# Kernel optimization log

Hardware: AMD Instinct MI355X
Metric: run time of the kernel (lower is better)

## Reference

```python
import jax, jax.numpy as jnp
import numpy as np

LN_EPS = 1e-5


def setup_inputs() -> dict:
    key = jax.random.key(0)
    ks = jax.random.split(key, 6)
    B, I, H = 16384, 512, 512
    x = jax.random.normal(ks[0], (B, I), dtype=jnp.float32)
    h_prev = jax.random.normal(ks[1], (B, H), dtype=jnp.float32)
    c_prev = jax.random.normal(ks[2], (B, H), dtype=jnp.float32)
    # packed gate weights in i|f|g|o order (equivalent to 8 separate matmuls)
    W_i = jax.random.normal(ks[3], (I, 4 * H), dtype=jnp.float32) * (1.0 / np.sqrt(I))
    W_h = jax.random.normal(ks[4], (H, 4 * H), dtype=jnp.float32) * (1.0 / np.sqrt(H))
    # biases: b_i=0, b_f=1, b_g=0, b_o=0 as in the torch module
    b = jnp.concatenate([jnp.zeros(H), jnp.ones(H), jnp.zeros(H), jnp.zeros(H)]).astype(jnp.float32)
    ln_weight = jnp.ones((H,), dtype=jnp.float32)
    ln_bias = jnp.zeros((H,), dtype=jnp.float32)
    return {"x": x, "h_prev": h_prev, "c_prev": c_prev, "W_i": W_i, "W_h": W_h,
            "b": b, "ln_weight": ln_weight, "ln_bias": ln_bias}


def layer_norm(h, w, bias):
    mu = jnp.mean(h, axis=-1, keepdims=True)
    var = jnp.var(h, axis=-1, keepdims=True)
    return (h - mu) * jax.lax.rsqrt(var + LN_EPS) * w + bias


def reference(x, h_prev, c_prev, W_i, W_h, b, ln_weight, ln_bias):
    H = h_prev.shape[-1]
    # two fused GEMMs covering all 4 gates: [B, 4H]
    gates = x @ W_i + h_prev @ W_h + b
    i, f, g, o = jnp.split(gates, 4, axis=-1)
    i = jax.nn.sigmoid(i)
    f = jax.nn.sigmoid(f)
    g = jnp.tanh(g)
    o = jax.nn.sigmoid(o)
    c = f * c_prev + i * g
    h = o * jnp.tanh(c)
    h = layer_norm(h, ln_weight, ln_bias)
    return (h, c)
```

## Files before the change

### kernel.cpp

```cpp
#include <hip/hip_runtime.h>
#include <cstdint>
#include <cstddef>

typedef unsigned short ushort_t;
typedef __attribute__((ext_vector_type(8))) short bf16x8;
typedef __attribute__((ext_vector_type(4))) float f32x4;

#define MROWS 16384
#define KDIM  1024
#define NDIM  2048
#define HDIM  512
#define NTILE 16

static __device__ __forceinline__ unsigned short f2bf(float f) {
    unsigned int u = __float_as_uint(f);
    u += 0x7fffu + ((u >> 16) & 1u);
    return (unsigned short)(u >> 16);
}

static __device__ __forceinline__ float sigmoid_f(float x) {
    return 1.0f / (1.0f + __expf(-x));
}
static __device__ __forceinline__ float tanh_f(float x) {
    float t = __expf(2.0f * x);
    return 1.0f - 2.0f / (t + 1.0f);
}

__global__ __launch_bounds__(256) void pack_ab(const float* __restrict__ x,
                                               const float* __restrict__ hp,
                                               const float* __restrict__ Wi,
                                               const float* __restrict__ Wh,
                                               ushort_t* __restrict__ A,
                                               ushort_t* __restrict__ Bt) {
    __shared__ ushort_t sm[64][72];
    const int tid = threadIdx.x;
    if (blockIdx.x < 8192) {
        int t = blockIdx.x * 256 + tid;
        int row = t >> 7;
        int kc = (t & 127) << 3;
        const float* src = (kc < 512) ? (x + (size_t)row * 512 + kc)
                                      : (hp + (size_t)row * 512 + (kc - 512));
        float4 v0 = ((const float4*)src)[0];
        float4 v1 = ((const float4*)src)[1];
        ushort_t o[8] __attribute__((aligned(16)));
        o[0] = f2bf(v0.x); o[1] = f2bf(v0.y); o[2] = f2bf(v0.z); o[3] = f2bf(v0.w);
        o[4] = f2bf(v1.x); o[5] = f2bf(v1.y); o[6] = f2bf(v1.z); o[7] = f2bf(v1.w);
        *((uint4*)(A + (size_t)row * KDIM + kc)) = *((const uint4*)o);
    } else {
        int b2 = blockIdx.x - 8192;
        int kt = b2 >> 5;
        int ct = b2 & 31;
        const float* W = (kt < 8) ? (Wi + (size_t)(kt * 64) * NDIM)
                                  : (Wh + (size_t)((kt - 8) * 64) * NDIM);
        int c0 = (tid & 15) * 4;
        int r0 = tid >> 4;
#pragma unroll
        for (int r = 0; r < 4; ++r) {
            int krow = r * 16 + r0;
            float4 v = *((const float4*)(W + (size_t)krow * NDIM + ct * 64 + c0));
            sm[krow][c0 + 0] = f2bf(v.x);
            sm[krow][c0 + 1] = f2bf(v.y);
            sm[krow][c0 + 2] = f2bf(v.z);
            sm[krow][c0 + 3] = f2bf(v.w);
        }
        __syncthreads();
        int g = (ct * 64) >> 9;
        int h0 = ct * 64 - g * 512;
#pragma unroll
        for (int q = tid; q < 512; q += 256) {
            int cc = q >> 3;
            int kc = (q & 7) * 8;
            ushort_t o[8] __attribute__((aligned(16)));
#pragma unroll
            for (int j = 0; j < 8; ++j) o[j] = sm[kc + j][cc];
            int np = 4 * (h0 + cc) + g;
            *((uint4*)(Bt + (size_t)np * KDIM + kt * 64 + kc)) = *((const uint4*)o);
        }
    }
}

__global__ __launch_bounds__(512, 2) void gemm_cell(const ushort_t* __restrict__ A,
                                                    const ushort_t* __restrict__ Bt,
                                                    const float* __restrict__ b,
                                                    const float* __restrict__ c_prev,
                                                    float* __restrict__ h_out,
                                                    float* __restrict__ c_out) {
    __shared__ ushort_t lds[2][32768];

    const int tid  = threadIdx.x;
    const int w    = tid >> 6;
    const int lane = tid & 63;
    const int mi   = w >> 2;
    const int nj   = w & 3;
    int bid = blockIdx.x;
    int lid = (bid & 7) * 64 + (bid >> 3);
    const int m0 = (lid >> 3) * 256;
    const int n0 = (lid & 7) * 256;
    const int lr   = lane & 15;
    const int quad = lane >> 4;
    const int sw   = lr & 7;

    const int trow0 = tid >> 3;
    const int chg   = (tid & 7) ^ (trow0 & 7);
    const size_t a_base = (size_t)(m0 + trow0) * KDIM + chg * 8;
    const size_t b_base = (size_t)(n0 + trow0) * KDIM + chg * 8;
    const int    l_base = tid * 16;

#define STAGE_A(kt, bufi) do {                                                      \
    const ushort_t* ap_ = A + a_base + (size_t)(kt) * 64;                           \
    char* al_ = (char*)&lds[bufi][0];                                               \
    _Pragma("unroll")                                                               \
    for (int r_ = 0; r_ < 4; ++r_)                                                  \
        __builtin_amdgcn_global_load_lds(                                           \
            (const __attribute__((address_space(1))) void*)(ap_ + (size_t)r_ * 64 * KDIM), \
            (__attribute__((address_space(3))) void*)(al_ + l_base + r_ * 8192),    \
            16, 0, 0);                                                              \
} while (0)
#define STAGE_B(kt, bufi) do {                                                      \
    const ushort_t* bp_ = Bt + b_base + (size_t)(kt) * 64;                          \
    char* bl_ = (char*)&lds[bufi][16384];                                           \
    _Pragma("unroll")                                                               \
    for (int r_ = 0; r_ < 4; ++r_)                                                  \
        __builtin_amdgcn_global_load_lds(                                           \
            (const __attribute__((address_space(1))) void*)(bp_ + (size_t)r_ * 64 * KDIM), \
            (__attribute__((address_space(3))) void*)(bl_ + l_base + r_ * 8192),    \
            16, 0, 0);                                                              \
} while (0)

    f32x4 acc[8][4];
#pragma unroll
    for (int i = 0; i < 8; ++i)
#pragma unroll
        for (int j = 0; j < 4; ++j) acc[i][j] = (f32x4){0.f, 0.f, 0.f, 0.f};

    STAGE_A(0, 0); STAGE_B(0, 0);
    STAGE_A(1, 1); STAGE_B(1, 1);
    asm volatile("s_waitcnt vmcnt(8)\n\ts_barrier" ::: "memory");

#define TILE(t_, BUF_) do {                                                         \
    const ushort_t* Ab_ = &lds[BUF_][0];                                            \
    const ushort_t* Bb_ = &lds[BUF_][16384];                                        \
    bf16x8 af[4][2], b0v[2][2], b1v[2][2];                                          \
                                 \
    _Pragma("unroll")                                                               \
    for (int t2 = 0; t2 < 4; ++t2) {                                                \
        int ra = mi * 128 + t2 * 16 + lr;                                           \
        af[t2][0] = *((const bf16x8*)(Ab_ + (ra * 8 + (quad ^ sw)) * 8));           \
        af[t2][1] = *((const bf16x8*)(Ab_ + (ra * 8 + ((4 + quad) ^ sw)) * 8));     \
    }                                                                               \
    _Pragma("unroll")                                                               \
    for (int j = 0; j < 2; ++j) {                                                   \
        int rb = nj * 64 + j * 16 + lr;                                             \
        b0v[j][0] = *((const bf16x8*)(Bb_ + (rb * 8 + (quad ^ sw)) * 8));           \
        b0v[j][1] = *((const bf16x8*)(Bb_ + (rb * 8 + ((4 + quad) ^ sw)) * 8));     \
    }                                                                               \
    __builtin_amdgcn_s_barrier();                                                   \
    __builtin_amdgcn_s_setprio(1);                                                  \
    _Pragma("unroll")                                                               \
    for (int t2 = 0; t2 < 4; ++t2)                                                  \
        _Pragma("unroll")                                                           \
        for (int j = 0; j < 2; ++j) {                                               \
            acc[t2][j] = __builtin_amdgcn_mfma_f32_16x16x32_bf16(                   \
                af[t2][0], b0v[j][0], acc[t2][j], 0, 0, 0);                         \
            acc[t2][j] = __builtin_amdgcn_mfma_f32_16x16x32_bf16(                   \
                af[t2][1], b0v[j][1], acc[t2][j], 0, 0, 0);                         \
        }                                                                           \
    __builtin_amdgcn_s_setprio(0);                                                  \
    asm volatile("s_barrier" ::: "memory");                                         \
                                        \
    _Pragma("unroll")                                                               \
    for (int j = 0; j < 2; ++j) {                                                   \
        int rb = nj * 64 + (j + 2) * 16 + lr;                                       \
        b1v[j][0] = *((const bf16x8*)(Bb_ + (rb * 8 + (quad ^ sw)) * 8));           \
        b1v[j][1] = *((const bf16x8*)(Bb_ + (rb * 8 + ((4 + quad) ^ sw)) * 8));     \
    }                                                                               \
    __builtin_amdgcn_s_barrier();                                                   \
    __builtin_amdgcn_s_setprio(1);                                                  \
    _Pragma("unroll")                                                               \
    for (int t2 = 0; t2 < 4; ++t2)                                                  \
        _Pragma("unroll")                                                           \
        for (int j = 0; j < 2; ++j) {                                               \
            acc[t2][j + 2] = __builtin_amdgcn_mfma_f32_16x16x32_bf16(               \
                af[t2][0], b1v[j][0], acc[t2][j + 2], 0, 0, 0);                     \
            acc[t2][j + 2] = __builtin_amdgcn_mfma_f32_16x16x32_bf16(               \
                af[t2][1], b1v[j][1], acc[t2][j + 2], 0, 0, 0);                     \
        }                                                                           \
    __builtin_amdgcn_s_setprio(0);                                                  \
    asm volatile("s_barrier" ::: "memory");          \
                         \
    _Pragma("unroll")                                                               \
    for (int t2 = 0; t2 < 4; ++t2) {                                                \
        int ra = mi * 128 + (t2 + 4) * 16 + lr;                                     \
        af[t2][0] = *((const bf16x8*)(Ab_ + (ra * 8 + (quad ^ sw)) * 8));           \
        af[t2][1] = *((const bf16x8*)(Ab_ + (ra * 8 + ((4 + quad) ^ sw)) * 8));     \
    }                                                                               \
    if ((t_) < NTILE - 2) STAGE_B((t_) + 2, BUF_);                                  \
    __builtin_amdgcn_s_barrier();                                                   \
    __builtin_amdgcn_s_setprio(1);                                                  \
    _Pragma("unroll")                                                               \
    for (int t2 = 0; t2 < 4; ++t2)                                                  \
        _Pragma("unroll")                                                           \
        for (int j = 0; j < 2; ++j) {                                               \
            acc[t2 + 4][j + 2] = __builtin_amdgcn_mfma_f32_16x16x32_bf16(           \
                af[t2][0], b1v[j][0], acc[t2 + 4][j + 2], 0, 0, 0);                 \
            acc[t2 + 4][j + 2] = __builtin_amdgcn_mfma_f32_16x16x32_bf16(           \
                af[t2][1], b1v[j][1], acc[t2 + 4][j + 2], 0, 0, 0);                 \
        }                                                                           \
    __builtin_amdgcn_s_setprio(0);                                                  \
    asm volatile("s_barrier" ::: "memory");          \
                            \
    if ((t_) < NTILE - 2) STAGE_A((t_) + 2, BUF_);                                  \
    __builtin_amdgcn_s_barrier();                                                   \
    __builtin_amdgcn_s_setprio(1);                                                  \
    _Pragma("unroll")                                                               \
    for (int t2 = 0; t2 < 4; ++t2)                                                  \
        _Pragma("unroll")                                                           \
        for (int j = 0; j < 2; ++j) {                                               \
            acc[t2 + 4][j] = __builtin_amdgcn_mfma_f32_16x16x32_bf16(               \
                af[t2][0], b0v[j][0], acc[t2 + 4][j], 0, 0, 0);                     \
            acc[t2 + 4][j] = __builtin_amdgcn_mfma_f32_16x16x32_bf16(               \
                af[t2][1], b0v[j][1], acc[t2 + 4][j], 0, 0, 0);                     \
        }                                                                           \
    __builtin_amdgcn_s_setprio(0);                                                  \
    if ((t_) < NTILE - 2) {                                                         \
                 \
        asm volatile("s_waitcnt vmcnt(8)\n\ts_barrier" ::: "memory");               \
    } else if ((t_) == NTILE - 2) {                                                 \
        asm volatile("s_waitcnt vmcnt(0)\n\ts_barrier" ::: "memory");               \
    } else {                                                                        \
        asm volatile("s_waitcnt lgkmcnt(0)\n\ts_barrier" ::: "memory");             \
    }                                                                               \
} while (0)

    for (int tp = 0; tp < NTILE / 2; ++tp) {
        TILE(2 * tp, 0);
        TILE(2 * tp + 1, 1);
    }
#undef TILE
#undef STAGE_A
#undef STAGE_B

    float* scr = (float*)&lds[0][0] + w * 1024;
    const int rr = lane >> 2;
    const int hg0 = ((n0 + nj * 64) >> 2) + (lane & 3) * 4;
    const float4 bi4 = *((const float4*)(b + hg0));
    const float4 bff = *((const float4*)(b + 512 + hg0));
    const float4 bgg = *((const float4*)(b + 1024 + hg0));
    const float4 boo = *((const float4*)(b + 1536 + hg0));
    const float bi[4] = {bi4.x, bi4.y, bi4.z, bi4.w};
    const float bfv[4] = {bff.x, bff.y, bff.z, bff.w};
    const float bg[4] = {bgg.x, bgg.y, bgg.z, bgg.w};
    const float bo[4] = {boo.x, boo.y, boo.z, boo.w};

#pragma unroll
    for (int tm = 0; tm < 8; ++tm) {
#pragma unroll
        for (int tn = 0; tn < 4; ++tn) {
            int c = tn * 16 + lr;
#pragma unroll
            for (int rg = 0; rg < 4; ++rg) {
                int r = quad * 4 + rg;
                int blk = (c >> 2) ^ r;
                scr[r * 64 + blk * 4 + (c & 3)] = acc[tm][tn][rg];
            }
        }
        float4 gv[4];
#pragma unroll
        for (int j = 0; j < 4; ++j) {
            int cb = (lane & 3) * 4 + j;
            gv[j] = *((const float4*)(scr + rr * 64 + (cb ^ rr) * 4));
        }
        int grow = m0 + mi * 128 + tm * 16 + rr;
        float4 cp4 = *((const float4*)(c_prev + (size_t)grow * HDIM + hg0));
        const float cpv[4] = {cp4.x, cp4.y, cp4.z, cp4.w};
        float cn[4], hv[4];
#pragma unroll
        for (int j = 0; j < 4; ++j) {
            float iv = sigmoid_f(gv[j].x + bi[j]);
            float fv = sigmoid_f(gv[j].y + bfv[j]);
            float g2 = tanh_f(gv[j].z + bg[j]);
            float ov = sigmoid_f(gv[j].w + bo[j]);
            cn[j] = fv * cpv[j] + iv * g2;
            hv[j] = ov * tanh_f(cn[j]);
        }
        float4 cno = {cn[0], cn[1], cn[2], cn[3]};
        float4 hvo = {hv[0], hv[1], hv[2], hv[3]};
        *((float4*)(c_out + (size_t)grow * HDIM + hg0)) = cno;
        *((float4*)(h_out + (size_t)grow * HDIM + hg0)) = hvo;
    }
}

__global__ __launch_bounds__(256) void ln_kernel(float* __restrict__ h,
                                                 const float* __restrict__ lw,
                                                 const float* __restrict__ lb) {
    int w = threadIdx.x >> 6;
    int lane = threadIdx.x & 63;
    int row = blockIdx.x * 4 + w;
    float* p = h + (size_t)row * HDIM + lane * 8;
    float4 a = ((const float4*)p)[0];
    float4 c = ((const float4*)p)[1];
    float s  = a.x + a.y + a.z + a.w + c.x + c.y + c.z + c.w;
    float ss = a.x * a.x + a.y * a.y + a.z * a.z + a.w * a.w +
               c.x * c.x + c.y * c.y + c.z * c.z + c.w * c.w;
#pragma unroll
    for (int off = 32; off > 0; off >>= 1) {
        s  += __shfl_xor(s, off);
        ss += __shfl_xor(ss, off);
    }
    float mu = s * (1.0f / 512.0f);
    float var = ss * (1.0f / 512.0f) - mu * mu;
    float rstd = rsqrtf(var + 1e-5f);
    const float* wp = lw + lane * 8;
    const float* bp = lb + lane * 8;
    float4 w0 = ((const float4*)wp)[0];
    float4 w1 = ((const float4*)wp)[1];
    float4 b0 = ((const float4*)bp)[0];
    float4 b1 = ((const float4*)bp)[1];
    a.x = (a.x - mu) * rstd * w0.x + b0.x;
    a.y = (a.y - mu) * rstd * w0.y + b0.y;
    a.z = (a.z - mu) * rstd * w0.z + b0.z;
    a.w = (a.w - mu) * rstd * w0.w + b0.w;
    c.x = (c.x - mu) * rstd * w1.x + b1.x;
    c.y = (c.y - mu) * rstd * w1.y + b1.y;
    c.z = (c.z - mu) * rstd * w1.z + b1.z;
    c.w = (c.w - mu) * rstd * w1.w + b1.w;
    ((float4*)p)[0] = a;
    ((float4*)p)[1] = c;
}

extern "C" void kernel_launch(void* const* d_in, const int* in_sizes, int n_in,
                              void* d_out, int out_size, void* d_ws, size_t ws_size,
                              hipStream_t stream) {
    const float* x      = (const float*)d_in[0];
    const float* h_prev = (const float*)d_in[1];
    const float* c_prev = (const float*)d_in[2];
    const float* W_i    = (const float*)d_in[3];
    const float* W_h    = (const float*)d_in[4];
    const float* b      = (const float*)d_in[5];
    const float* ln_w   = (const float*)d_in[6];
    const float* ln_b   = (const float*)d_in[7];

    float* h_out = (float*)d_out;
    float* c_out = h_out + (size_t)MROWS * HDIM;

    ushort_t* A  = (ushort_t*)d_ws;
    ushort_t* Bt = A + (size_t)MROWS * KDIM;

    pack_ab<<<8192 + 512, 256, 0, stream>>>(x, h_prev, W_i, W_h, A, Bt);
    gemm_cell<<<512, 512, 0, stream>>>(A, Bt, b, c_prev, h_out, c_out);
    ln_kernel<<<MROWS / 4, 256, 0, stream>>>(h_out, ln_w, ln_b);
}
```

Baseline: 246.6 us.

## Split LDS staging into per-slot loads interleaved across MFMA phases, drop barriers

Breaks the A and B global-to-LDS staging into individual 64-row slots. Each slot is issued as soon as all waves have finished reading that slot from the current buffer, so the prefetch spreads across the four MFMA phases instead of arriving in two bursts. Several s_barrier calls between LDS fragment reads and the MFMA blocks are removed to cut synchronisation stalls. The risk is that correctness now depends on exactly which slots each wave reads in each phase, and the scheduling of the prefetch traffic changes.

```diff
diff --git a/kernel.cpp b/kernel.cpp
--- a/kernel.cpp
+++ b/kernel.cpp
@@ -106,26 +106,18 @@
     const size_t b_base = (size_t)(n0 + trow0) * KDIM + chg * 8;
     const int    l_base = tid * 16;
 
-#define STAGE_A(kt, bufi) do {                                                      \
-    const ushort_t* ap_ = A + a_base + (size_t)(kt) * 64;                           \
-    char* al_ = (char*)&lds[bufi][0];                                               \
-    _Pragma("unroll")                                                               \
-    for (int r_ = 0; r_ < 4; ++r_)                                                  \
-        __builtin_amdgcn_global_load_lds(                                           \
-            (const __attribute__((address_space(1))) void*)(ap_ + (size_t)r_ * 64 * KDIM), \
-            (__attribute__((address_space(3))) void*)(al_ + l_base + r_ * 8192),    \
-            16, 0, 0);                                                              \
-} while (0)
-#define STAGE_B(kt, bufi) do {                                                      \
-    const ushort_t* bp_ = Bt + b_base + (size_t)(kt) * 64;                          \
-    char* bl_ = (char*)&lds[bufi][16384];                                           \
-    _Pragma("unroll")                                                               \
-    for (int r_ = 0; r_ < 4; ++r_)                                                  \
-        __builtin_amdgcn_global_load_lds(                                           \
-            (const __attribute__((address_space(1))) void*)(bp_ + (size_t)r_ * 64 * KDIM), \
-            (__attribute__((address_space(3))) void*)(bl_ + l_base + r_ * 8192),    \
-            16, 0, 0);                                                              \
-} while (0)
+#define STAGE_A_SLOT(kt, bufi, r_)                                              \
+    __builtin_amdgcn_global_load_lds(                                           \
+        (const __attribute__((address_space(1))) void*)(A + a_base +            \
+            (size_t)(kt) * 64 + (size_t)(r_) * 64 * KDIM),                      \
+        (__attribute__((address_space(3))) void*)((char*)&lds[bufi][0] +        \
+            l_base + (r_) * 8192), 16, 0, 0)
+#define STAGE_B_SLOT(kt, bufi, r_)                                              \
+    __builtin_amdgcn_global_load_lds(                                           \
+        (const __attribute__((address_space(1))) void*)(Bt + b_base +           \
+            (size_t)(kt) * 64 + (size_t)(r_) * 64 * KDIM),                      \
+        (__attribute__((address_space(3))) void*)((char*)&lds[bufi][16384] +    \
+            l_base + (r_) * 8192), 16, 0, 0)
 
     f32x4 acc[8][4];
 #pragma unroll
@@ -133,15 +125,17 @@
 #pragma unroll
         for (int j = 0; j < 4; ++j) acc[i][j] = (f32x4){0.f, 0.f, 0.f, 0.f};
 
-    STAGE_A(0, 0); STAGE_B(0, 0);
-    STAGE_A(1, 1); STAGE_B(1, 1);
+    STAGE_A_SLOT(0, 0, 0); STAGE_A_SLOT(0, 0, 1); STAGE_A_SLOT(0, 0, 2); STAGE_A_SLOT(0, 0, 3);
+    STAGE_B_SLOT(0, 0, 0); STAGE_B_SLOT(0, 0, 1); STAGE_B_SLOT(0, 0, 2); STAGE_B_SLOT(0, 0, 3);
+    STAGE_A_SLOT(1, 1, 0); STAGE_A_SLOT(1, 1, 1); STAGE_A_SLOT(1, 1, 2); STAGE_A_SLOT(1, 1, 3);
+    STAGE_B_SLOT(1, 1, 0); STAGE_B_SLOT(1, 1, 1); STAGE_B_SLOT(1, 1, 2); STAGE_B_SLOT(1, 1, 3);
     asm volatile("s_waitcnt vmcnt(8)\n\ts_barrier" ::: "memory");
 
 #define TILE(t_, BUF_) do {                                                         \
     const ushort_t* Ab_ = &lds[BUF_][0];                                            \
     const ushort_t* Bb_ = &lds[BUF_][16384];                                        \
     bf16x8 af[4][2], b0v[2][2], b1v[2][2];                                          \
-                                 \
+                    \
     _Pragma("unroll")                                                               \
     for (int t2 = 0; t2 < 4; ++t2) {                                                \
         int ra = mi * 128 + t2 * 16 + lr;                                           \
@@ -154,7 +148,6 @@
         b0v[j][0] = *((const bf16x8*)(Bb_ + (rb * 8 + (quad ^ sw)) * 8));           \
         b0v[j][1] = *((const bf16x8*)(Bb_ + (rb * 8 + ((4 + quad) ^ sw)) * 8));     \
     }                                                                               \
-    __builtin_amdgcn_s_barrier();                                                   \
     __builtin_amdgcn_s_setprio(1);                                                  \
     _Pragma("unroll")                                                               \
     for (int t2 = 0; t2 < 4; ++t2)                                                  \
@@ -166,15 +159,16 @@
                 af[t2][1], b0v[j][1], acc[t2][j], 0, 0, 0);                         \
         }                                                                           \
     __builtin_amdgcn_s_setprio(0);                                                  \
-    asm volatile("s_barrier" ::: "memory");                                         \
-                                        \
+    asm volatile("s_barrier" ::: "memory");           \
+    if ((t_) < NTILE - 2) { STAGE_A_SLOT((t_) + 2, BUF_, 0);                        \
+                            STAGE_A_SLOT((t_) + 2, BUF_, 2); }                      \
+                                            \
     _Pragma("unroll")                                                               \
     for (int j = 0; j < 2; ++j) {                                                   \
         int rb = nj * 64 + (j + 2) * 16 + lr;                                       \
         b1v[j][0] = *((const bf16x8*)(Bb_ + (rb * 8 + (quad ^ sw)) * 8));           \
         b1v[j][1] = *((const bf16x8*)(Bb_ + (rb * 8 + ((4 + quad) ^ sw)) * 8));     \
     }                                                                               \
-    __builtin_amdgcn_s_barrier();                                                   \
     __builtin_amdgcn_s_setprio(1);                                                  \
     _Pragma("unroll")                                                               \
     for (int t2 = 0; t2 < 4; ++t2)                                                  \
@@ -186,16 +180,33 @@
                 af[t2][1], b1v[j][1], acc[t2][j + 2], 0, 0, 0);                     \
         }                                                                           \
     __builtin_amdgcn_s_setprio(0);                                                  \
-    asm volatile("s_barrier" ::: "memory");          \
-                         \
+    asm volatile("s_barrier" ::: "memory");            \
+    if ((t_) < NTILE - 2) { STAGE_B_SLOT((t_) + 2, BUF_, 0);                        \
+                            STAGE_B_SLOT((t_) + 2, BUF_, 1); }                      \
+          \
     _Pragma("unroll")                                                               \
     for (int t2 = 0; t2 < 4; ++t2) {                                                \
         int ra = mi * 128 + (t2 + 4) * 16 + lr;                                     \
         af[t2][0] = *((const bf16x8*)(Ab_ + (ra * 8 + (quad ^ sw)) * 8));           \
         af[t2][1] = *((const bf16x8*)(Ab_ + (ra * 8 + ((4 + quad) ^ sw)) * 8));     \
     }                                                                               \
-    if ((t_) < NTILE - 2) STAGE_B((t_) + 2, BUF_);                                  \
-    __builtin_amdgcn_s_barrier();                                                   \
+    __builtin_amdgcn_s_setprio(1);                                                  \
+    _Pragma("unroll")                                                               \
+    for (int t2 = 0; t2 < 4; ++t2)                                                  \
+        _Pragma("unroll")                                                           \
+        for (int j = 0; j < 2; ++j) {                                               \
+            acc[t2 + 4][j] = __builtin_amdgcn_mfma_f32_16x16x32_bf16(               \
+                af[t2][0], b0v[j][0], acc[t2 + 4][j], 0, 0, 0);                     \
+            acc[t2 + 4][j] = __builtin_amdgcn_mfma_f32_16x16x32_bf16(               \
+                af[t2][1], b0v[j][1], acc[t2 + 4][j], 0, 0, 0);                     \
+        }                                                                           \
+    __builtin_amdgcn_s_setprio(0);                                                  \
+    asm volatile("s_waitcnt lgkmcnt(0)\n\ts_barrier" ::: "memory");         \
+    if ((t_) < NTILE - 2) { STAGE_B_SLOT((t_) + 2, BUF_, 2);                        \
+                            STAGE_B_SLOT((t_) + 2, BUF_, 3);                        \
+                            STAGE_A_SLOT((t_) + 2, BUF_, 1);                        \
+                            STAGE_A_SLOT((t_) + 2, BUF_, 3); }                      \
+               \
     __builtin_amdgcn_s_setprio(1);                                                  \
     _Pragma("unroll")                                                               \
     for (int t2 = 0; t2 < 4; ++t2)                                                  \
@@ -207,23 +218,8 @@
                 af[t2][1], b1v[j][1], acc[t2 + 4][j + 2], 0, 0, 0);                 \
         }                                                                           \
     __builtin_amdgcn_s_setprio(0);                                                  \
-    asm volatile("s_barrier" ::: "memory");          \
-                            \
-    if ((t_) < NTILE - 2) STAGE_A((t_) + 2, BUF_);                                  \
-    __builtin_amdgcn_s_barrier();                                                   \
-    __builtin_amdgcn_s_setprio(1);                                                  \
-    _Pragma("unroll")                                                               \
-    for (int t2 = 0; t2 < 4; ++t2)                                                  \
-        _Pragma("unroll")                                                           \
-        for (int j = 0; j < 2; ++j) {                                               \
-            acc[t2 + 4][j] = __builtin_amdgcn_mfma_f32_16x16x32_bf16(               \
-                af[t2][0], b0v[j][0], acc[t2 + 4][j], 0, 0, 0);                     \
-            acc[t2 + 4][j] = __builtin_amdgcn_mfma_f32_16x16x32_bf16(               \
-                af[t2][1], b0v[j][1], acc[t2 + 4][j], 0, 0, 0);                     \
-        }                                                                           \
-    __builtin_amdgcn_s_setprio(0);                                                  \
     if ((t_) < NTILE - 2) {                                                         \
-                 \
+             \
         asm volatile("s_waitcnt vmcnt(8)\n\ts_barrier" ::: "memory");               \
     } else if ((t_) == NTILE - 2) {                                                 \
         asm volatile("s_waitcnt vmcnt(0)\n\ts_barrier" ::: "memory");               \
@@ -237,8 +233,8 @@
         TILE(2 * tp + 1, 1);
     }
 #undef TILE
-#undef STAGE_A
-#undef STAGE_B
+#undef STAGE_A_SLOT
+#undef STAGE_B_SLOT
 
     float* scr = (float*)&lds[0][0] + w * 1024;
     const int rr = lane >> 2;
```

Result: no change. 245.2 us (-0.6%).
